# Kernel optimization log

Hardware: AMD Instinct MI355X
Metric: run time of the kernel (lower is better)

## Reference

```python
import jax, jax.numpy as jnp
import numpy as np

EMBED_DIM = 768
ATTN_DIM = 64


def setup_inputs() -> dict:
    key = jax.random.key(0)
    k1, k2, k3, k4 = jax.random.split(key, 4)
    embedded = jax.random.normal(k1, (4, 4096, EMBED_DIM), dtype=jnp.float32)
    scale = 1.0 / np.sqrt(EMBED_DIM)
    Wq = jax.random.normal(k2, (EMBED_DIM, ATTN_DIM), dtype=jnp.float32) * scale
    Wk = jax.random.normal(k3, (EMBED_DIM, ATTN_DIM), dtype=jnp.float32) * scale
    Wv = jax.random.normal(k4, (EMBED_DIM, ATTN_DIM), dtype=jnp.float32) * scale
    return {"embedded": embedded, "Wq": Wq, "Wk": Wk, "Wv": Wv}


def reference(embedded, Wq, Wk, Wv):
    # Linear projections (bias=False): [B, S, A]
    q = jnp.einsum("bse,ea->bsa", embedded, Wq)
    k = jnp.einsum("bse,ea->bsa", embedded, Wk)
    v = jnp.einsum("bse,ea->bsa", embedded, Wv)
    # Full [B, S, S] score matrix, as in the original naive implementation
    scores = jnp.einsum("bqa,bka->bqk", q, k) / jnp.sqrt(jnp.float32(ATTN_DIM))
    seq_len = embedded.shape[-2]
    causal = jnp.tril(jnp.ones((seq_len, seq_len), dtype=bool))
    scores = jnp.where(causal, scores, -jnp.inf)
    weights = jax.nn.softmax(scores, axis=-1)
    output = jnp.einsum("bqk,bka->bqa", weights, v)
    # torch.round(output, decimals=4)
    return jnp.round(output * 1e4) / 1e4
```

## Files before the change

kernel.cpp:

```cpp
#include <hip/hip_runtime.h>

#define NB 4
#define SEQ 4096
#define EMB 768
#define AD 64
#define BS (NB*SEQ)
#define CHK 16

typedef short short8 __attribute__((ext_vector_type(8)));
typedef float f32x4 __attribute__((ext_vector_type(4)));
typedef int   i32x2 __attribute__((ext_vector_type(2)));
typedef unsigned short u16;

__device__ __forceinline__ u16 f2bf(float f) {
  union { float f; unsigned u; } v; v.f = f;
  unsigned u = v.u;
  unsigned r = (u + 0x7FFFu + ((u >> 16) & 1u)) >> 16;
  return (u16)r;
}

__device__ __forceinline__ unsigned cvt_pk_bf16(float lo, float hi) {
  unsigned r;
  asm("v_cvt_pk_bf16_f32 %0, %1, %2" : "=v"(r) : "v"(lo), "v"(hi));
  return r;
}

__device__ __forceinline__ f32x4 mfma16(short8 a, short8 b, f32x4 c) {
  return __builtin_amdgcn_mfma_f32_16x16x32_bf16(a, b, c, 0, 0, 0);
}

__device__ __forceinline__ void gload16(const u16* g, u16* l) {
  __builtin_amdgcn_global_load_lds(
      (const __attribute__((address_space(1))) unsigned*)g,
      (__attribute__((address_space(3))) unsigned*)l, 16, 0, 0);
}

__device__ __forceinline__ float xor16_max(float x) {
#if __has_builtin(__builtin_amdgcn_permlane16_swap)
  i32x2 r = __builtin_amdgcn_permlane16_swap(__float_as_int(x), __float_as_int(x), false, false);
  return fmaxf(__int_as_float(r[0]), __int_as_float(r[1]));
#else
  return fmaxf(x, __shfl_xor(x, 16));
#endif
}
__device__ __forceinline__ float xor16_sum(float x) {
#if __has_builtin(__builtin_amdgcn_permlane16_swap)
  i32x2 r = __builtin_amdgcn_permlane16_swap(__float_as_int(x), __float_as_int(x), false, false);
  return __int_as_float(r[0]) + __int_as_float(r[1]);
#else
  return x + __shfl_xor(x, 16);
#endif
}
__device__ __forceinline__ float xor32_max(float x) {
#if __has_builtin(__builtin_amdgcn_permlane32_swap)
  i32x2 r = __builtin_amdgcn_permlane32_swap(__float_as_int(x), __float_as_int(x), false, false);
  return fmaxf(__int_as_float(r[0]), __int_as_float(r[1]));
#else
  return fmaxf(x, __shfl_xor(x, 32));
#endif
}
__device__ __forceinline__ float xor32_sum(float x) {
#if __has_builtin(__builtin_amdgcn_permlane32_swap)
  i32x2 r = __builtin_amdgcn_permlane32_swap(__float_as_int(x), __float_as_int(x), false, false);
  return __int_as_float(r[0]) + __int_as_float(r[1]);
#else
  return x + __shfl_xor(x, 32);
#endif
}

__global__ void wt_kernel(const float* __restrict__ Wq, const float* __restrict__ Wk,
                          const float* __restrict__ Wv, u16* __restrict__ Wt) {
  int idx = blockIdx.x * 256 + threadIdx.x;
  if (idx >= 3 * AD * EMB) return;
  int m   = idx / (AD * EMB);
  int rem = idx - m * (AD * EMB);
  int col = rem / EMB;
  int e   = rem - col * EMB;
  const float* W = (m == 0) ? Wq : (m == 1) ? Wk : Wv;
  Wt[idx] = f2bf(W[e * AD + col]);
}

__global__ __launch_bounds__(512) void proj_kernel(const float* __restrict__ emb,
                                                   const u16* __restrict__ Wt,
                                                   u16* __restrict__ Q, u16* __restrict__ K,
                                                   u16* __restrict__ Vt) {
  const int w = threadIdx.x >> 6;
  const int lane = threadIdx.x & 63;
  const int g = lane >> 4, c = lane & 15;
  const int wr = w & 1;
  const int cq = w >> 1;
  const int rbase = blockIdx.x * 32;

  __shared__ __align__(16) char ebuf[2][2][4096];
  __shared__ __align__(16) char wbuf[2][2][12288];
  __shared__ u16 t[32][65];

  const int r8 = lane >> 3, j8 = lane & 7;
  const int c4 = lane >> 2, j4 = lane & 3;

  f32x4 acc[3];
#pragma unroll
  for (int fi = 0; fi < 3; ++fi)
#pragma unroll
    for (int r = 0; r < 4; ++r) acc[fi][r] = 0.f;

#define PSTAGE(bufi, kk, kt) do {                                              \
    { const int col = w * 16 + c4;                                             \
      const int kc = (col & 3) ^ ((col >> 2) & 3);                             \
      gload16(Wt + (size_t)col * EMB + (kt) * 32 + ((j4 ^ kc) << 3),           \
              (u16*)(wbuf[bufi][kk] + w * 1024)); }                            \
    if (w < 4) {                                                               \
      gload16((const u16*)(emb + (size_t)(rbase + w * 8 + r8) * EMB            \
                           + (kt) * 32 + ((j8 ^ r8) << 2)),                    \
              (u16*)(ebuf[bufi][kk] + w * 1024));                              \
    } else {                                                                   \
      const int col = (4 + w) * 16 + c4;                                       \
      const int kc = (col & 3) ^ ((col >> 2) & 3);                             \
      gload16(Wt + (size_t)col * EMB + (kt) * 32 + ((j4 ^ kc) << 3),           \
              (u16*)(wbuf[bufi][kk] + (4 + w) * 1024));                        \
    }                                                                          \
  } while (0)

  PSTAGE(0, 0, 0);
  PSTAGE(0, 1, 1);
  __syncthreads();

  int cur = 0;
  for (int it = 0; it < 12; ++it) {
    if (it + 1 < 12) {
      PSTAGE(cur ^ 1, 0, 2 * it + 2);
      PSTAGE(cur ^ 1, 1, 2 * it + 3);
    }

#pragma unroll
    for (int kk = 0; kk < 2; ++kk) {
      const char* eb = ebuf[cur][kk];
      const int arow = (wr * 16 + c) * 128;
      const int sw = (c & 7) << 4;
      float4 fa0 = *(const float4*)(eb + arow + ((g * 32) ^ sw));
      float4 fa1 = *(const float4*)(eb + arow + ((g * 32 + 16) ^ sw));
      short8 af;
      af[0] = (short)f2bf(fa0.x); af[1] = (short)f2bf(fa0.y);
      af[2] = (short)f2bf(fa0.z); af[3] = (short)f2bf(fa0.w);
      af[4] = (short)f2bf(fa1.x); af[5] = (short)f2bf(fa1.y);
      af[6] = (short)f2bf(fa1.z); af[7] = (short)f2bf(fa1.w);

      const char* wb = wbuf[cur][kk];
#pragma unroll
      for (int fi = 0; fi < 3; ++fi) {
        const int fg = cq * 3 + fi;
        const int col = (fg >> 2) * 64 + (fg & 3) * 16 + c;
        const int kc = (col & 3) ^ ((col >> 2) & 3);
        short8 bf = *(const short8*)(wb + col * 64 + ((g ^ kc) << 4));
        acc[fi] = mfma16(af, bf, acc[fi]);
      }
    }

    __syncthreads();
    cur ^= 1;
  }

#pragma unroll
  for (int fi = 0; fi < 3; ++fi) {
    const int fg = cq * 3 + fi;
    const int m = fg >> 2, cf = fg & 3;
    const int col = cf * 16 + c;
#pragma unroll
    for (int r = 0; r < 4; ++r) {
      const int rloc = wr * 16 + g * 4 + r;
      const size_t grow = (size_t)(rbase + rloc);
      const float v = acc[fi][r];
      if (m == 0)      Q[grow * AD + col] = f2bf(v * 0.125f);
      else if (m == 1) K[grow * AD + col] = f2bf(v);
      else             t[rloc][col] = f2bf(v);
    }
  }
  __syncthreads();
  const int bb = blockIdx.x >> 7;
  const int sb = (blockIdx.x & 127) * 32;
  const int s = threadIdx.x & 31;
  const int d0 = threadIdx.x >> 5;
#pragma unroll
  for (int it = 0; it < 4; ++it) {
    const int d = it * 16 + d0;
    Vt[(size_t)(bb * AD + d) * SEQ + sb + s] = t[s][d];
  }
#undef PSTAGE
}

__global__ __launch_bounds__(256, 3) void flash_part(const u16* __restrict__ Q,
                                                     const u16* __restrict__ K,
                                                     const u16* __restrict__ Vt,
                                                     float* __restrict__ opart,
                                                     float* __restrict__ ml) {
  const int bx = blockIdx.x;
  const int b = bx & 3;
  const int u = bx >> 2;
  int bq, c;
  if (u < 16)       { bq = 16 + u;        c = 0; }
  else if (u < 32)  { bq = 32 + (u - 16); c = 0; }
  else if (u < 48)  { bq = 32 + (u - 32); c = 1; }
  else if (u < 64)  { bq = 48 + (u - 48); c = 0; }
  else if (u < 80)  { bq = 48 + (u - 64); c = 1; }
  else if (u < 96)  { bq = 48 + (u - 80); c = 2; }
  else { int d = u - 96; bq = (d >> 4) * 16 + 15 - (d & 15); c = d >> 4; }
  const int t0 = c * CHK;
  const int tend = (c == (bq >> 4)) ? (bq + 1) : (t0 + CHK);

  const int w = threadIdx.x >> 6;
  const int lane = threadIdx.x & 63;
  const int g = lane >> 4, cl = lane & 15;
  const int r8 = lane >> 3, c16 = lane & 7;
  const int q0 = bq * 64 + w * 16;

  const u16* Qb = Q + (size_t)b * SEQ * AD;
  const u16* Kb = K + (size_t)b * SEQ * AD;
  const u16* Vb = Vt + (size_t)b * AD * SEQ;

  __shared__ __align__(16) u16 kbuf[2][64 * 64];
  __shared__ __align__(16) u16 vbuf[2][64 * 64];
  __shared__ __align__(16) u16 plds_all[4][16 * 64];
  char* plds = (char*)plds_all[w];
  const int swz = (cl & 7) << 4;
  const int prow = cl * 128;
  const int fsw = (cl & 7);

  const short8 qf0 = *(const short8*)(Qb + (size_t)(q0 + cl) * AD + g * 8);
  const short8 qf1 = *(const short8*)(Qb + (size_t)(q0 + cl) * AD + 32 + g * 8);

  float mrow = -INFINITY, lrow = 0.f;
  f32x4 o[4];
#pragma unroll
  for (int cf = 0; cf < 4; cf++)
#pragma unroll
    for (int r = 0; r < 4; r++) o[cf][r] = 0.f;

#define STAGE(bufi, tt) do {                                                   \
    const int kvb = (tt) * 64;                                                 \
    const int row0 = w * 16 + r8, row1 = w * 16 + 8 + r8;                      \
    gload16(Kb + (size_t)(kvb + row0) * AD + ((c16 ^ r8) << 3),                \
            &kbuf[bufi][(w * 16) * 64]);                                       \
    gload16(Kb + (size_t)(kvb + row1) * AD + ((c16 ^ r8) << 3),                \
            &kbuf[bufi][(w * 16 + 8) * 64]);                                   \
    gload16(Vb + (size_t)row0 * SEQ + kvb + ((c16 ^ r8) << 3),                 \
            &vbuf[bufi][(w * 16) * 64]);                                       \
    gload16(Vb + (size_t)row1 * SEQ + kvb + ((c16 ^ r8) << 3),                 \
            &vbuf[bufi][(w * 16 + 8) * 64]);                                   \
  } while (0)

  STAGE(0, t0);
  __syncthreads();

  int cur = 0;
  for (int t = t0; t < tend; ++t) {
    const int kv0 = t * 64;
    if (t + 1 < tend) STAGE(cur ^ 1, t + 1);

    const char* kb = (const char*)kbuf[cur];
    const char* vb = (const char*)vbuf[cur];

    short8 kf0[4], kf1[4];
#pragma unroll
    for (int cf = 0; cf < 4; cf++) {
      const int kr = (cf * 16 + cl) * 128;
      kf0[cf] = *(const short8*)(kb + kr + ((g ^ fsw) << 4));
      kf1[cf] = *(const short8*)(kb + kr + (((4 + g) ^ fsw) << 4));
    }

    f32x4 s4[4];
#pragma unroll
    for (int cf = 0; cf < 4; cf++) {
      f32x4 z; z[0] = z[1] = z[2] = z[3] = 0.f;
      z = mfma16(kf0[cf], qf0, z);
      s4[cf] = mfma16(kf1[cf], qf1, z);
    }

    if (t == bq) {
#pragma unroll
      for (int cf = 0; cf < 4; cf++) {
        const int kvb2 = kv0 + cf * 16 + g * 4;
#pragma unroll
        for (int r = 0; r < 4; r++)
          s4[cf][r] = (kvb2 + r <= q0 + cl) ? s4[cf][r] : -INFINITY;
      }
    }

    float tm[4];
#pragma unroll
    for (int cf = 0; cf < 4; cf++)
      tm[cf] = fmaxf(fmaxf(s4[cf][0], s4[cf][1]), fmaxf(s4[cf][2], s4[cf][3]));
    float mt = fmaxf(fmaxf(tm[0], tm[1]), fmaxf(tm[2], tm[3]));
    mt = xor16_max(mt);
    mt = xor32_max(mt);

    if (!__all(mt <= mrow + 8.0f)) {
      const float mn = fmaxf(mrow, mt);
      const float corr = __expf(mrow - mn);
      mrow = mn;
      lrow *= corr;
      float cb[4];
#pragma unroll
      for (int r = 0; r < 4; r++) cb[r] = __shfl(corr, g * 20 + r);
#pragma unroll
      for (int cf = 0; cf < 4; cf++) {
        o[cf][0] *= cb[0]; o[cf][1] *= cb[1];
        o[cf][2] *= cb[2]; o[cf][3] *= cb[3];
      }
    }

    float rs = 0.f;
#pragma unroll
    for (int cf = 0; cf < 4; cf++) {
      const float p0 = __expf(s4[cf][0] - mrow);
      const float p1 = __expf(s4[cf][1] - mrow);
      const float p2 = __expf(s4[cf][2] - mrow);
      const float p3 = __expf(s4[cf][3] - mrow);
      rs += (p0 + p1) + (p2 + p3);
      uint2 val;
      val.x = cvt_pk_bf16(p0, p1);
      val.y = cvt_pk_bf16(p2, p3);
      *(uint2*)(plds + prow + (((cf * 32) + (g * 8)) ^ swz)) = val;
    }
    rs = xor16_sum(rs);
    rs = xor32_sum(rs);
    lrow += rs;

    asm volatile("" ::: "memory");

#pragma unroll
    for (int f = 0; f < 2; ++f) {
      const short8 pf = *(const short8*)(plds + prow + ((f * 64 + g * 16) ^ swz));
#pragma unroll
      for (int cf = 0; cf < 4; cf++) {
        const int vr = (cf * 16 + cl) * 128;
        const short8 vfa = *(const short8*)(vb + vr + (((f * 4 + g) ^ fsw) << 4));
        o[cf] = mfma16(pf, vfa, o[cf]);
      }
    }

    __syncthreads();
    cur ^= 1;
  }

  const int qg = bq * 4 + w;
  const int k2 = qg >> 6;
  const int slot = b * 640 + 32 * k2 * (k2 + 1) + (qg & 63) * (k2 + 1) + c;

  if (lane < 16) {
    ml[(size_t)slot * 32 + cl * 2 + 0] = mrow;
    ml[(size_t)slot * 32 + cl * 2 + 1] = lrow;
  }
#pragma unroll
  for (int cf = 0; cf < 4; cf++)
#pragma unroll
    for (int r = 0; r < 4; r++)
      opart[(size_t)slot * 1024 + (g * 4 + r) * 64 + cf * 16 + cl] = o[cf][r];
#undef STAGE
}

__global__ __launch_bounds__(256) void combine_kernel(const float* __restrict__ opart,
                                                      const float* __restrict__ ml,
                                                      float* __restrict__ out) {
  const int tid = threadIdx.x;
  const int row = blockIdx.x * 16 + (tid >> 4);
  const int d = (tid & 15) * 4;
  const int b = row >> 12;
  const int rowb = row & 4095;
  const int qg = rowb >> 4;
  const int r = rowb & 15;
  const int k2 = qg >> 6;
  const int nc = k2 + 1;
  const int sbase = b * 640 + 32 * k2 * (k2 + 1) + (qg & 63) * nc;

  float M = -INFINITY;
  float ms[4], ls[4];
  for (int cc = 0; cc < nc; cc++) {
    ms[cc] = ml[(size_t)(sbase + cc) * 32 + r * 2 + 0];
    ls[cc] = ml[(size_t)(sbase + cc) * 32 + r * 2 + 1];
    M = fmaxf(M, ms[cc]);
  }
  float L = 0.f;
  float4 acc = {0.f, 0.f, 0.f, 0.f};
  for (int cc = 0; cc < nc; cc++) {
    const float wgt = __expf(ms[cc] - M);
    L += ls[cc] * wgt;
    float4 ov = *(const float4*)(opart + (size_t)(sbase + cc) * 1024 + r * 64 + d);
    acc.x += ov.x * wgt; acc.y += ov.y * wgt;
    acc.z += ov.z * wgt; acc.w += ov.w * wgt;
  }
  const float inv = 1.0f / L;
  float4 res;
  res.x = rintf(acc.x * inv * 1.0e4f) * 1.0e-4f;
  res.y = rintf(acc.y * inv * 1.0e4f) * 1.0e-4f;
  res.z = rintf(acc.z * inv * 1.0e4f) * 1.0e-4f;
  res.w = rintf(acc.w * inv * 1.0e4f) * 1.0e-4f;
  *(float4*)(out + (size_t)row * AD + d) = res;
}

extern "C" void kernel_launch(void* const* d_in, const int* in_sizes, int n_in,
                              void* d_out, int out_size, void* d_ws, size_t ws_size,
                              hipStream_t stream) {
  const float* emb = (const float*)d_in[0];
  const float* Wq  = (const float*)d_in[1];
  const float* Wk  = (const float*)d_in[2];
  const float* Wv  = (const float*)d_in[3];
  float* out = (float*)d_out;

  char* ws = (char*)d_ws;
  u16* Wt = (u16*)ws;
  u16* Q  = (u16*)(ws + 294912);
  u16* K  = Q + (size_t)BS * AD;
  u16* Vt = K + (size_t)BS * AD;
  float* opart = (float*)(ws + 294912 + 3 * (size_t)BS * AD * 2);
  float* ml    = opart + (size_t)2560 * 1024;

  wt_kernel<<<(3 * AD * EMB + 255) / 256, 256, 0, stream>>>(Wq, Wk, Wv, Wt);
  proj_kernel<<<BS / 32, 512, 0, stream>>>(emb, Wt, Q, K, Vt);
  flash_part<<<640, 256, 0, stream>>>(Q, K, Vt, opart, ml);
  combine_kernel<<<BS / 16, 256, 0, stream>>>(opart, ml, out);
}
```

Measured before the change: 58.96 us.

## Store partial attention outputs in bf16 and use packed bf16 conversion

The partial output accumulators written by the flash kernel and read by the combine kernel are now stored as bf16 instead of fp32, halving that intermediate traffic. Separately, the projection kernel converts fp32 embeddings to bf16 with the packed hardware instruction instead of manual per-element rounding. Storing partials in bf16 loses precision before the combine and the 1e-4 rounding, which risks output mismatches.

```diff
diff --git a/kernel.cpp b/kernel.cpp
--- a/kernel.cpp
+++ b/kernel.cpp
@@ -17,6 +17,11 @@
   unsigned u = v.u;
   unsigned r = (u + 0x7FFFu + ((u >> 16) & 1u)) >> 16;
   return (u16)r;
+}
+
+__device__ __forceinline__ float bf2f(u16 b) {
+  union { unsigned u; float f; } v; v.u = ((unsigned)b) << 16;
+  return v.f;
 }
 
 __device__ __forceinline__ unsigned cvt_pk_bf16(float lo, float hi) {
@@ -139,11 +144,12 @@
       const int sw = (c & 7) << 4;
       float4 fa0 = *(const float4*)(eb + arow + ((g * 32) ^ sw));
       float4 fa1 = *(const float4*)(eb + arow + ((g * 32 + 16) ^ sw));
-      short8 af;
-      af[0] = (short)f2bf(fa0.x); af[1] = (short)f2bf(fa0.y);
-      af[2] = (short)f2bf(fa0.z); af[3] = (short)f2bf(fa0.w);
-      af[4] = (short)f2bf(fa1.x); af[5] = (short)f2bf(fa1.y);
-      af[6] = (short)f2bf(fa1.z); af[7] = (short)f2bf(fa1.w);
+      union { unsigned u[4]; short8 v; } uu;
+      uu.u[0] = cvt_pk_bf16(fa0.x, fa0.y);
+      uu.u[1] = cvt_pk_bf16(fa0.z, fa0.w);
+      uu.u[2] = cvt_pk_bf16(fa1.x, fa1.y);
+      uu.u[3] = cvt_pk_bf16(fa1.z, fa1.w);
+      const short8 af = uu.v;
 
       const char* wb = wbuf[cur][kk];
 #pragma unroll
@@ -191,7 +197,7 @@
 __global__ __launch_bounds__(256, 3) void flash_part(const u16* __restrict__ Q,
                                                      const u16* __restrict__ K,
                                                      const u16* __restrict__ Vt,
-                                                     float* __restrict__ opart,
+                                                     u16* __restrict__ opart,
                                                      float* __restrict__ ml) {
   const int bx = blockIdx.x;
   const int b = bx & 3;
@@ -354,11 +360,11 @@
   for (int cf = 0; cf < 4; cf++)
 #pragma unroll
     for (int r = 0; r < 4; r++)
-      opart[(size_t)slot * 1024 + (g * 4 + r) * 64 + cf * 16 + cl] = o[cf][r];
+      opart[(size_t)slot * 1024 + (g * 4 + r) * 64 + cf * 16 + cl] = f2bf(o[cf][r]);
 #undef STAGE
 }
 
-__global__ __launch_bounds__(256) void combine_kernel(const float* __restrict__ opart,
+__global__ __launch_bounds__(256) void combine_kernel(const u16* __restrict__ opart,
                                                       const float* __restrict__ ml,
                                                       float* __restrict__ out) {
   const int tid = threadIdx.x;
@@ -384,9 +390,9 @@
   for (int cc = 0; cc < nc; cc++) {
     const float wgt = __expf(ms[cc] - M);
     L += ls[cc] * wgt;
-    float4 ov = *(const float4*)(opart + (size_t)(sbase + cc) * 1024 + r * 64 + d);
-    acc.x += ov.x * wgt; acc.y += ov.y * wgt;
-    acc.z += ov.z * wgt; acc.w += ov.w * wgt;
+    ushort4 ov = *(const ushort4*)(opart + (size_t)(sbase + cc) * 1024 + r * 64 + d);
+    acc.x += bf2f(ov.x) * wgt; acc.y += bf2f(ov.y) * wgt;
+    acc.z += bf2f(ov.z) * wgt; acc.w += bf2f(ov.w) * wgt;
   }
   const float inv = 1.0f / L;
   float4 res;
@@ -411,8 +417,9 @@
   u16* Q  = (u16*)(ws + 294912);
   u16* K  = Q + (size_t)BS * AD;
   u16* Vt = K + (size_t)BS * AD;
-  float* opart = (float*)(ws + 294912 + 3 * (size_t)BS * AD * 2);
-  float* ml    = opart + (size_t)2560 * 1024;
+  u16* opart = (u16*)(ws + 294912 + 3 * (size_t)BS * AD * 2);
+  float* ml  = (float*)(ws + 294912 + 3 * (size_t)BS * AD * 2
+                        + (size_t)2560 * 1024 * 2);
 
   wt_kernel<<<(3 * AD * EMB + 255) / 256, 256, 0, stream>>>(Wq, Wk, Wv, Wt);
   proj_kernel<<<BS / 32, 512, 0, stream>>>(emb, Wt, Q, K, Vt);
```

Result: no change. 57.95 us (-1.7%).
